# Optimization experiments

Measured on AMD Instinct MI355X. Metric: run time of the kernel, lower is better.

The kernel has to match this reference:

```python
import jax, jax.numpy as jnp
import numpy as np

N_EMBD = 1024
N_HEAD = 16
HEAD_DIM = N_EMBD // N_HEAD  # 64; scale = sqrt(64) = 8


def setup_inputs() -> dict:
    key = jax.random.key(0)
    k0, k1, k2, k3, k4 = jax.random.split(key, 5)
    B, T = 4, 2048
    x = jax.random.normal(k0, (B, T, N_EMBD), dtype=jnp.float32)
    # torch Linear weights are (out,in); we store (in,out) so y = x @ W + b
    W_attn = jax.random.normal(k1, (N_EMBD, 3 * N_EMBD), dtype=jnp.float32) * 0.02
    b_attn = jax.random.normal(k2, (3 * N_EMBD,), dtype=jnp.float32) * 0.02
    W_proj = jax.random.normal(k3, (N_EMBD, N_EMBD), dtype=jnp.float32) * 0.02
    b_proj = jax.random.normal(k4, (N_EMBD,), dtype=jnp.float32) * 0.02
    return {"x": x, "W_attn": W_attn, "b_attn": b_attn,
            "W_proj": W_proj, "b_proj": b_proj}


def reference(x, W_attn, b_attn, W_proj, b_proj):
    B, T, D = x.shape
    scale = 1.0 / np.float32(np.sqrt(HEAD_DIM))
    qkv = x @ W_attn + b_attn                      # [B,T,3D]
    q, k, v = jnp.split(qkv, 3, axis=-1)           # each [B,T,D]
    att = jnp.einsum('bid,bjd->bij', q, k) * scale # [B,T,T]
    causal = jnp.tril(jnp.ones((T, T), dtype=bool))
    att = jnp.where(causal[None, :, :], att, jnp.float32(-jnp.inf))
    att = jax.nn.softmax(att, axis=-1)
    y = jnp.einsum('bij,bjd->bid', att, v)         # [B,T,D]
    return y @ W_proj + b_proj
```

## Files before the change

### kernel.cpp

```cpp
#include <hip/hip_runtime.h>

typedef __attribute__((ext_vector_type(8))) short short8;
typedef __attribute__((ext_vector_type(4))) float f32x4;
typedef __attribute__((ext_vector_type(4))) unsigned short ushort4v;

struct DB0 { static constexpr int value = 0; };
struct DB1 { static constexpr int value = 1; };

__device__ __forceinline__ unsigned short f2bf(float f) {
  unsigned int u = __float_as_uint(f);
  u += 0x7fffu + ((u >> 16) & 1u);
  return (unsigned short)(u >> 16);
}
__device__ __forceinline__ float bf2f(unsigned short h) {
  return __uint_as_float(((unsigned int)h) << 16);
}

__device__ __forceinline__ void gload16(const unsigned short* g, unsigned short* l) {
  __builtin_amdgcn_global_load_lds(
      (const __attribute__((address_space(1))) unsigned int*)g,
      (__attribute__((address_space(3))) unsigned int*)l,
      16, 0, 0);
}

template <int OFF>
__device__ __forceinline__ short8 dsr(unsigned a) {
  short8 r;
  asm volatile("ds_read_b128 %0, %1 offset:%2" : "=v"(r) : "v"(a), "n"(OFF));
  return r;
}

__device__ __forceinline__ void bar() {
  asm volatile("" ::: "memory");
  __builtin_amdgcn_s_barrier();
  asm volatile("" ::: "memory");
}

__global__ __launch_bounds__(256) void prep_kernel(
    const float* __restrict__ x, unsigned short* __restrict__ xb,
    const float* __restrict__ Wa, unsigned short* __restrict__ wta,
    const float* __restrict__ Wp, unsigned short* __restrict__ wtp) {
  int b = blockIdx.x;
  int tx = threadIdx.x & 31, ty = threadIdx.x >> 5;
  if (b < 8192) {
    int i = b * 256 + threadIdx.x;
    f32x4 v = ((const f32x4*)x)[i];
    ushort4v o;
    o[0] = f2bf(v[0]); o[1] = f2bf(v[1]); o[2] = f2bf(v[2]); o[3] = f2bf(v[3]);
    ((ushort4v*)xb)[i] = o;
    return;
  }
  const float* W; unsigned short* Wt; int K, N, n0, k0;
  if (b < 8192 + 3072) {
    int bb = b - 8192; W = Wa; Wt = wta; K = 1024; N = 3072;
    n0 = (bb % 96) * 32; k0 = (bb / 96) * 32;
  } else {
    int bb = b - 11264; W = Wp; Wt = wtp; K = 1024; N = 1024;
    n0 = (bb % 32) * 32; k0 = (bb / 32) * 32;
  }
  __shared__ float tile[32][33];
#pragma unroll
  for (int j = 0; j < 32; j += 8)
    tile[ty + j][tx] = W[(size_t)(k0 + ty + j) * N + n0 + tx];
  __syncthreads();
#pragma unroll
  for (int j = 0; j < 32; j += 8)
    Wt[(size_t)(n0 + ty + j) * K + k0 + tx] = f2bf(tile[tx][ty + j]);
}

__global__ __launch_bounds__(256) void softmax_kernel(unsigned short* __restrict__ S) {
  int row = blockIdx.x * 4 + (threadIdx.x >> 6);
  int l = threadIdx.x & 63;
  int rl = row & 2047;
  int rend = ((rl >> 7) + 1) << 7;
  unsigned short* p = S + (size_t)row * 2048;
  float v[32];
  float mx = -3e38f;
#pragma unroll
  for (int i = 0; i < 4; i++) {
    int c0 = (i * 64 + l) * 8;
    if (c0 < rend) {
      short8 raw = *(const short8*)&p[c0];
#pragma unroll
      for (int j = 0; j < 8; j++) {
        v[i * 8 + j] = bf2f((unsigned short)raw[j]);
        mx = fmaxf(mx, v[i * 8 + j]);
      }
    } else {
#pragma unroll
      for (int j = 0; j < 8; j++) v[i * 8 + j] = -3e38f;
    }
  }
#pragma unroll
  for (int off = 1; off < 64; off <<= 1) mx = fmaxf(mx, __shfl_xor(mx, off));
  float s = 0.f;
#pragma unroll
  for (int i = 0; i < 32; i++) { v[i] = exp2f((v[i] - mx) * 1.44269504f); s += v[i]; }
#pragma unroll
  for (int off = 1; off < 64; off <<= 1) s += __shfl_xor(s, off);
  float inv = 1.f / s;
#pragma unroll
  for (int i = 0; i < 4; i++) {
    int c0 = (i * 64 + l) * 8;
    if (c0 < rend) {
      short8 o;
#pragma unroll
      for (int j = 0; j < 8; j++) o[j] = (short)f2bf(v[i * 8 + j] * inv);
      *(short8*)&p[c0] = o;
    }
  }
}

template <int OUTBF>
__global__ __launch_bounds__(256) void gemm128_kernel(
    const unsigned short* __restrict__ A, int lda, long long saz,
    const unsigned short* __restrict__ Bt, int ldb, long long sbz,
    void* __restrict__ Cv, int ldc, long long scz,
    const float* __restrict__ bias, int K, float scale, int causal) {
  __shared__ __align__(16) unsigned short lds[2][16384];

  int bx, by, z;
  if (causal == 4) {
    int gx = gridDim.x, gy = gridDim.y, gz = gridDim.z;
    int total = gx * gy * gz;
    int id = blockIdx.x + blockIdx.y * gx + blockIdx.z * gx * gy;
    int halfn = total >> 1;
    int half = id >= halfn;
    int r = id - half * halfn;
    bx = r % gx;
    int rest = r / gx;
    int by0 = rest % gy;
    z = rest / gy + half * (gz >> 1);
    by = half ? (gy - 1 - by0) : by0;
  } else {
    bx = blockIdx.x; by = blockIdx.y; z = blockIdx.z;
  }
  const int m0 = by * 128, n0 = bx * 128;
  A += (size_t)z * saz;
  Bt += (size_t)z * sbz;

  const int t = threadIdx.x;
  const int lane = t & 63, wid = t >> 6;
  const int g = lane >> 4, q = lane & 15;
  const int wm = wid >> 1, wn = wid & 1;

  int NT = K >> 6;
  if (causal == 1) {
    if (n0 >= m0 + 128) return;
  } else if (causal == 4) {
    NT = min(K, m0 + 128) >> 6;
  }

  f32x4 acc[4][4] = {};

  {
    const int scol = ((t & 7) * 8) ^ ((t & 32) >> 1);
    const unsigned short* aS = A + (size_t)(m0 + (t >> 3)) * lda + scol;
    const unsigned short* bS = Bt + (size_t)(n0 + (t >> 3)) * ldb + scol;

    auto stage = [&](int tt) {
      unsigned short* d = &lds[tt & 1][wid * 512];
      const unsigned short* sa = aS + (size_t)tt * 64;
      const unsigned short* sb = bS + (size_t)tt * 64;
      gload16(sa, d);
      gload16(sa + (size_t)32 * lda, d + 2048);
      gload16(sa + (size_t)64 * lda, d + 4096);
      gload16(sa + (size_t)96 * lda, d + 6144);
      gload16(sb, d + 8192);
      gload16(sb + (size_t)32 * ldb, d + 10240);
      gload16(sb + (size_t)64 * ldb, d + 12288);
      gload16(sb + (size_t)96 * ldb, d + 14336);
    };

    const unsigned base =
        (unsigned)(unsigned long long)(__attribute__((address_space(3))) unsigned short*)&lds[0][0];
    const int colA = (g * 16) ^ ((q & 4) << 3);
    const unsigned aaB = base + (unsigned)((wm * 64 + q) * 128 + colA);
    const unsigned bbB = base + 16384u + (unsigned)((wn * 64 + q) * 128 + colA);

    stage(0);
    asm volatile("s_waitcnt vmcnt(0)" ::: "memory");
    bar();

    auto body = [&](auto dbc, int tt) {
      constexpr int DB = decltype(dbc)::value;
      const unsigned aa = aaB + DB * 32768u;
      const unsigned bb = bbB + DB * 32768u;
      if (tt + 1 < NT) stage(tt + 1);
      short8 aq[4][2], bq[4][2];
#pragma unroll
      for (int m = 0; m < 4; m++) {
        aq[m][0] = dsr<0>(aa + m * 2048u);
        aq[m][1] = dsr<64>(aa + m * 2048u);
      }
#pragma unroll
      for (int n = 0; n < 4; n++) {
        bq[n][0] = dsr<0>(bb + n * 2048u);
        bq[n][1] = dsr<64>(bb + n * 2048u);
      }
      asm volatile("s_waitcnt lgkmcnt(0)" ::: "memory");
      __builtin_amdgcn_sched_barrier(0);
      __builtin_amdgcn_s_setprio(1);
#pragma unroll
      for (int ks = 0; ks < 2; ks++)
#pragma unroll
        for (int m = 0; m < 4; m++)
#pragma unroll
          for (int n = 0; n < 4; n++)
            acc[m][n] = __builtin_amdgcn_mfma_f32_16x16x32_bf16(aq[m][ks], bq[n][ks], acc[m][n], 0, 0, 0);
      __builtin_amdgcn_s_setprio(0);
      __builtin_amdgcn_sched_barrier(0);
      asm volatile("s_waitcnt vmcnt(0)" ::: "memory");
      bar();
    };

    int tt = 0;
    for (; tt + 2 <= NT; tt += 2) {
      body(DB0{}, tt);
      body(DB1{}, tt + 1);
    }
    if (tt < NT) body(DB0{}, tt);
  }

  const bool maskC = (causal == 1);
#pragma unroll
  for (int n = 0; n < 4; n++) {
    int colg = n0 + wn * 64 + n * 16 + q;
    float bv = bias ? bias[colg] : 0.f;
#pragma unroll
    for (int m = 0; m < 4; m++) {
      int rowb = m0 + wm * 64 + m * 16 + g * 4;
#pragma unroll
      for (int r = 0; r < 4; r++) {
        float val = acc[m][n][r] * scale + bv;
        if (maskC && colg > rowb + r) val = -1e30f;
        if (OUTBF) {
          ((unsigned short*)Cv)[(size_t)z * scz + (size_t)(rowb + r) * ldc + colg] = f2bf(val);
        } else {
          ((float*)Cv)[(size_t)z * scz + (size_t)(rowb + r) * ldc + colg] = val;
        }
      }
    }
  }
}

extern "C" void kernel_launch(void* const* d_in, const int* in_sizes, int n_in,
                              void* d_out, int out_size, void* d_ws, size_t ws_size,
                              hipStream_t stream) {
  const float* x  = (const float*)d_in[0];
  const float* Wa = (const float*)d_in[1];
  const float* ba = (const float*)d_in[2];
  const float* Wp = (const float*)d_in[3];
  const float* bp = (const float*)d_in[4];
  float* out = (float*)d_out;

  char* ws = (char*)d_ws;
  unsigned short* qkv = (unsigned short*)(ws);
  unsigned short* xb  = (unsigned short*)(ws + 50331648);
  unsigned short* vt  = (unsigned short*)(ws + 50331648);
  unsigned short* wta = (unsigned short*)(ws + 67108864);
  unsigned short* S   = (unsigned short*)(ws + 73400320);
  unsigned short* wtp = (unsigned short*)(ws + 123731968);

  prep_kernel<<<12288, 256, 0, stream>>>(x, xb, Wa, wta, Wp, wtp);

  gemm128_kernel<1><<<dim3(24, 64, 1), 256, 0, stream>>>(
      xb, 1024, 0, wta, 1024, 0, qkv, 3072, 0, ba, 1024, 1.0f, 0);

  gemm128_kernel<1><<<dim3(16, 16, 4), 256, 0, stream>>>(
      qkv, 3072, 2048LL * 3072, qkv + 1024, 3072, 2048LL * 3072,
      S, 2048, 2048LL * 2048, nullptr, 1024, 0.125f, 1);

  softmax_kernel<<<2048, 256, 0, stream>>>(S);

  gemm128_kernel<1><<<dim3(16, 8, 4), 256, 0, stream>>>(
      wtp, 1024, 0, qkv + 2048, 3072, 2048LL * 3072,
      vt, 2048, 2048LL * 1024, nullptr, 1024, 1.0f, 0);

  gemm128_kernel<0><<<dim3(8, 16, 4), 256, 0, stream>>>(
      S, 2048, 2048LL * 2048, vt, 2048, 2048LL * 1024,
      out, 1024, 2048LL * 1024, bp, 2048, 1.0f, 4);
}
```

Baseline: 187.5 us.

## Merge QK^T scores and V-projection GEMMs into one triangular-grid launch

Extracts the GEMM tile body into a device function and adds a combined kernel that runs the V·Wproj transpose GEMM (512 tiles) and the causal QK^T score GEMM in a single launch. The score part now enumerates only lower-triangular tiles (136 per batch) instead of launching the full 16x16 grid and early-exiting. This removes one kernel launch and the idle blocks of the causal grid, and lets the two independent GEMMs fill the GPU together. The cost is a small sqrt-based triangular index decode per block.

```diff
diff --git a/kernel.cpp b/kernel.cpp
--- a/kernel.cpp
+++ b/kernel.cpp
@@ -112,13 +112,117 @@
 }
 
 template <int OUTBF>
+__device__ __forceinline__ void gemm_body(
+    unsigned short (*lds)[16384],
+    const unsigned short* __restrict__ A, int lda,
+    const unsigned short* __restrict__ Bt, int ldb,
+    void* __restrict__ Cv, int ldc,
+    const float* __restrict__ bias, int NT, float scale, bool maskC,
+    int m0, int n0) {
+  const int t = threadIdx.x;
+  const int lane = t & 63, wid = t >> 6;
+  const int g = lane >> 4, q = lane & 15;
+  const int wm = wid >> 1, wn = wid & 1;
+
+  f32x4 acc[4][4] = {};
+
+  {
+    const int scol = ((t & 7) * 8) ^ ((t & 32) >> 1);
+    const unsigned short* aS = A + (size_t)(m0 + (t >> 3)) * lda + scol;
+    const unsigned short* bS = Bt + (size_t)(n0 + (t >> 3)) * ldb + scol;
+
+    auto stage = [&](int tt) {
+      unsigned short* d = &lds[tt & 1][wid * 512];
+      const unsigned short* sa = aS + (size_t)tt * 64;
+      const unsigned short* sb = bS + (size_t)tt * 64;
+      gload16(sa, d);
+      gload16(sa + (size_t)32 * lda, d + 2048);
+      gload16(sa + (size_t)64 * lda, d + 4096);
+      gload16(sa + (size_t)96 * lda, d + 6144);
+      gload16(sb, d + 8192);
+      gload16(sb + (size_t)32 * ldb, d + 10240);
+      gload16(sb + (size_t)64 * ldb, d + 12288);
+      gload16(sb + (size_t)96 * ldb, d + 14336);
+    };
+
+    const unsigned base =
+        (unsigned)(unsigned long long)(__attribute__((address_space(3))) unsigned short*)&lds[0][0];
+    const int colA = (g * 16) ^ ((q & 4) << 3);
+    const unsigned aaB = base + (unsigned)((wm * 64 + q) * 128 + colA);
+    const unsigned bbB = base + 16384u + (unsigned)((wn * 64 + q) * 128 + colA);
+
+    stage(0);
+    asm volatile("s_waitcnt vmcnt(0)" ::: "memory");
+    bar();
+
+    auto body = [&](auto dbc, int tt) {
+      constexpr int DB = decltype(dbc)::value;
+      const unsigned aa = aaB + DB * 32768u;
+      const unsigned bb = bbB + DB * 32768u;
+      if (tt + 1 < NT) stage(tt + 1);
+      short8 aq[4][2], bq[4][2];
+#pragma unroll
+      for (int m = 0; m < 4; m++) {
+        aq[m][0] = dsr<0>(aa + m * 2048u);
+        aq[m][1] = dsr<64>(aa + m * 2048u);
+      }
+#pragma unroll
+      for (int n = 0; n < 4; n++) {
+        bq[n][0] = dsr<0>(bb + n * 2048u);
+        bq[n][1] = dsr<64>(bb + n * 2048u);
+      }
+      asm volatile("s_waitcnt lgkmcnt(0)" ::: "memory");
+      __builtin_amdgcn_sched_barrier(0);
+      __builtin_amdgcn_s_setprio(1);
+#pragma unroll
+      for (int ks = 0; ks < 2; ks++)
+#pragma unroll
+        for (int m = 0; m < 4; m++)
+#pragma unroll
+          for (int n = 0; n < 4; n++)
+            acc[m][n] = __builtin_amdgcn_mfma_f32_16x16x32_bf16(aq[m][ks], bq[n][ks], acc[m][n], 0, 0, 0);
+      __builtin_amdgcn_s_setprio(0);
+      __builtin_amdgcn_sched_barrier(0);
+      asm volatile("s_waitcnt vmcnt(0)" ::: "memory");
+      bar();
+    };
+
+    int tt = 0;
+    for (; tt + 2 <= NT; tt += 2) {
+      body(DB0{}, tt);
+      body(DB1{}, tt + 1);
+    }
+    if (tt < NT) body(DB0{}, tt);
+  }
+
+#pragma unroll
+  for (int n = 0; n < 4; n++) {
+    int colg = n0 + wn * 64 + n * 16 + q;
+    float bv = bias ? bias[colg] : 0.f;
+#pragma unroll
+    for (int m = 0; m < 4; m++) {
+      int rowb = m0 + wm * 64 + m * 16 + g * 4;
+#pragma unroll
+      for (int r = 0; r < 4; r++) {
+        float val = acc[m][n][r] * scale + bv;
+        if (maskC && colg > rowb + r) val = -1e30f;
+        if (OUTBF) {
+          ((unsigned short*)Cv)[(size_t)(rowb + r) * ldc + colg] = f2bf(val);
+        } else {
+          ((float*)Cv)[(size_t)(rowb + r) * ldc + colg] = val;
+        }
+      }
+    }
+  }
+}
+
+template <int OUTBF>
 __global__ __launch_bounds__(256) void gemm128_kernel(
     const unsigned short* __restrict__ A, int lda, long long saz,
     const unsigned short* __restrict__ Bt, int ldb, long long sbz,
     void* __restrict__ Cv, int ldc, long long scz,
     const float* __restrict__ bias, int K, float scale, int causal) {
   __shared__ __align__(16) unsigned short lds[2][16384];
-
   int bx, by, z;
   if (causal == 4) {
     int gx = gridDim.x, gy = gridDim.y, gz = gridDim.z;
@@ -136,111 +240,37 @@
     bx = blockIdx.x; by = blockIdx.y; z = blockIdx.z;
   }
   const int m0 = by * 128, n0 = bx * 128;
-  A += (size_t)z * saz;
-  Bt += (size_t)z * sbz;
-
-  const int t = threadIdx.x;
-  const int lane = t & 63, wid = t >> 6;
-  const int g = lane >> 4, q = lane & 15;
-  const int wm = wid >> 1, wn = wid & 1;
-
   int NT = K >> 6;
-  if (causal == 1) {
-    if (n0 >= m0 + 128) return;
-  } else if (causal == 4) {
-    NT = min(K, m0 + 128) >> 6;
-  }
-
-  f32x4 acc[4][4] = {};
-
-  {
-    const int scol = ((t & 7) * 8) ^ ((t & 32) >> 1);
-    const unsigned short* aS = A + (size_t)(m0 + (t >> 3)) * lda + scol;
-    const unsigned short* bS = Bt + (size_t)(n0 + (t >> 3)) * ldb + scol;
-
-    auto stage = [&](int tt) {
-      unsigned short* d = &lds[tt & 1][wid * 512];
-      const unsigned short* sa = aS + (size_t)tt * 64;
-      const unsigned short* sb = bS + (size_t)tt * 64;
-      gload16(sa, d);
-      gload16(sa + (size_t)32 * lda, d + 2048);
-      gload16(sa + (size_t)64 * lda, d + 4096);
-      gload16(sa + (size_t)96 * lda, d + 6144);
-      gload16(sb, d + 8192);
-      gload16(sb + (size_t)32 * ldb, d + 10240);
-      gload16(sb + (size_t)64 * ldb, d + 12288);
-      gload16(sb + (size_t)96 * ldb, d + 14336);
-    };
-
-    const unsigned base =
-        (unsigned)(unsigned long long)(__attribute__((address_space(3))) unsigned short*)&lds[0][0];
-    const int colA = (g * 16) ^ ((q & 4) << 3);
-    const unsigned aaB = base + (unsigned)((wm * 64 + q) * 128 + colA);
-    const unsigned bbB = base + 16384u + (unsigned)((wn * 64 + q) * 128 + colA);
-
-    stage(0);
-    asm volatile("s_waitcnt vmcnt(0)" ::: "memory");
-    bar();
-
-    auto body = [&](auto dbc, int tt) {
-      constexpr int DB = decltype(dbc)::value;
-      const unsigned aa = aaB + DB * 32768u;
-      const unsigned bb = bbB + DB * 32768u;
-      if (tt + 1 < NT) stage(tt + 1);
-      short8 aq[4][2], bq[4][2];
-#pragma unroll
-      for (int m = 0; m < 4; m++) {
-        aq[m][0] = dsr<0>(aa + m * 2048u);
-        aq[m][1] = dsr<64>(aa + m * 2048u);
-      }
-#pragma unroll
-      for (int n = 0; n < 4; n++) {
-        bq[n][0] = dsr<0>(bb + n * 2048u);
-        bq[n][1] = dsr<64>(bb + n * 2048u);
-      }
-      asm volatile("s_waitcnt lgkmcnt(0)" ::: "memory");
-      __builtin_amdgcn_sched_barrier(0);
-      __builtin_amdgcn_s_setprio(1);
-#pragma unroll
-      for (int ks = 0; ks < 2; ks++)
-#pragma unroll
-        for (int m = 0; m < 4; m++)
-#pragma unroll
-          for (int n = 0; n < 4; n++)
-            acc[m][n] = __builtin_amdgcn_mfma_f32_16x16x32_bf16(aq[m][ks], bq[n][ks], acc[m][n], 0, 0, 0);
-      __builtin_amdgcn_s_setprio(0);
-      __builtin_amdgcn_sched_barrier(0);
-      asm volatile("s_waitcnt vmcnt(0)" ::: "memory");
-      bar();
-    };
-
-    int tt = 0;
-    for (; tt + 2 <= NT; tt += 2) {
-      body(DB0{}, tt);
-      body(DB1{}, tt + 1);
-    }
-    if (tt < NT) body(DB0{}, tt);
-  }
-
-  const bool maskC = (causal == 1);
-#pragma unroll
-  for (int n = 0; n < 4; n++) {
-    int colg = n0 + wn * 64 + n * 16 + q;
-    float bv = bias ? bias[colg] : 0.f;
-#pragma unroll
-    for (int m = 0; m < 4; m++) {
-      int rowb = m0 + wm * 64 + m * 16 + g * 4;
-#pragma unroll
-      for (int r = 0; r < 4; r++) {
-        float val = acc[m][n][r] * scale + bv;
-        if (maskC && colg > rowb + r) val = -1e30f;
-        if (OUTBF) {
-          ((unsigned short*)Cv)[(size_t)z * scz + (size_t)(rowb + r) * ldc + colg] = f2bf(val);
-        } else {
-          ((float*)Cv)[(size_t)z * scz + (size_t)(rowb + r) * ldc + colg] = val;
-        }
-      }
-    }
+  if (causal == 4) NT = min(K, m0 + 128) >> 6;
+  char* C = (char*)Cv + (size_t)z * scz * (OUTBF ? 2 : 4);
+  gemm_body<OUTBF>(lds, A + (size_t)z * saz, lda, Bt + (size_t)z * sbz, ldb,
+                   C, ldc, bias, NT, scale, false, m0, n0);
+}
+
+__global__ __launch_bounds__(256) void gemm_sv_kernel(
+    const unsigned short* __restrict__ qkv,
+    const unsigned short* __restrict__ wtp,
+    unsigned short* __restrict__ S,
+    unsigned short* __restrict__ vt) {
+  __shared__ __align__(16) unsigned short lds[2][16384];
+  int i = blockIdx.x;
+  if (i < 512) {
+    int bx = i & 15, by = (i >> 4) & 7, z = i >> 7;
+    gemm_body<1>(lds, wtp, 1024,
+                 qkv + 2048 + (size_t)z * 2048 * 3072, 3072,
+                 vt + (size_t)z * 1024 * 2048, 2048,
+                 nullptr, 16, 1.0f, false, by * 128, bx * 128);
+  } else {
+    int ii = i - 512;
+    int z = ii / 136, tri = ii % 136;
+    int by = (int)((sqrtf(8.f * tri + 1.f) - 1.f) * 0.5f);
+    while ((by + 1) * (by + 2) / 2 <= tri) by++;
+    while (by * (by + 1) / 2 > tri) by--;
+    int bx = tri - by * (by + 1) / 2;
+    gemm_body<1>(lds, qkv + (size_t)z * 2048 * 3072, 3072,
+                 qkv + 1024 + (size_t)z * 2048 * 3072, 3072,
+                 S + (size_t)z * 2048 * 2048, 2048,
+                 nullptr, 16, 0.125f, true, by * 128, bx * 128);
   }
 }
 
@@ -267,15 +297,9 @@
   gemm128_kernel<1><<<dim3(24, 64, 1), 256, 0, stream>>>(
       xb, 1024, 0, wta, 1024, 0, qkv, 3072, 0, ba, 1024, 1.0f, 0);
 
-  gemm128_kernel<1><<<dim3(16, 16, 4), 256, 0, stream>>>(
-      qkv, 3072, 2048LL * 3072, qkv + 1024, 3072, 2048LL * 3072,
-      S, 2048, 2048LL * 2048, nullptr, 1024, 0.125f, 1);
+  gemm_sv_kernel<<<1056, 256, 0, stream>>>(qkv, wtp, S, vt);
 
   softmax_kernel<<<2048, 256, 0, stream>>>(S);
-
-  gemm128_kernel<1><<<dim3(16, 8, 4), 256, 0, stream>>>(
-      wtp, 1024, 0, qkv + 2048, 3072, 2048LL * 3072,
-      vt, 2048, 2048LL * 1024, nullptr, 1024, 1.0f, 0);
 
   gemm128_kernel<0><<<dim3(8, 16, 4), 256, 0, stream>>>(
       S, 2048, 2048LL * 2048, vt, 2048, 2048LL * 1024,
```

New measurement: 185.1 us. About the same (-1.3%).
